# Kernel tuning notes

Hardware: AMD Instinct MI355X
Metric: run time of the kernel (lower is better)

Reference implementation:

```python
import jax, jax.numpy as jnp
import numpy as np

NUM_HEADS = 12

def quick_gelu(z):
    return z * jax.nn.sigmoid(1.702 * z)

def setup_inputs() -> dict:
    key = jax.random.key(0)
    ks = jax.random.split(key, 8)
    B, Fn, P, E, R = 16, 12, 197, 768, 8
    s = 0.02
    return {
        "x": jax.random.normal(ks[0], (B * Fn, P, E), jnp.float32),
        "in_proj_weight": jax.random.normal(ks[1], (3 * E, E), jnp.float32) * s,
        "in_proj_bias": jnp.zeros((3 * E,), jnp.float32),
        "out_proj_weight": jax.random.normal(ks[2], (E, E), jnp.float32) * s,
        "out_proj_bias": jnp.zeros((E,), jnp.float32),
        "lora_a": jax.random.normal(ks[3], (R, E), jnp.float32) * s,
        "lora_b": jax.random.normal(ks[4], (3 * E, R), jnp.float32) * s,
        "down_w": jax.random.normal(ks[5], (R, E), jnp.float32) * s,
        "down_b": jnp.zeros((R,), jnp.float32),
        "up_w": jax.random.normal(ks[6], (E, R), jnp.float32) * s,
        "up_b": jnp.zeros((E,), jnp.float32),
        "b": B, "n_f": Fn, "token_len": P, "d_v": E,
    }

def reference(x, in_proj_weight, in_proj_bias, out_proj_weight, out_proj_bias,
              lora_a, lora_b, down_w, down_b, up_w, up_b,
              b, n_f, token_len, d_v):
    bsz, tgt, E = x.shape
    h = NUM_HEADS
    hd = E // h
    scaling = float(hd) ** -0.5

    # fused qkv + LoRA delta: [bsz, tgt, 3E]
    qkv = x @ in_proj_weight.T + in_proj_bias
    qkv = qkv + (x @ lora_a.T) @ lora_b.T
    qkv = qkv.reshape(bsz, tgt, 3, h, hd).transpose(2, 0, 3, 1, 4)
    q, k, v = qkv[0], qkv[1], qkv[2]  # each [bsz, h, tgt, hd]

    # CLS-token query per frame: (b f) h p d -> b h f d  (p=0)
    q_1 = q.reshape(b, n_f, h, tgt, hd).transpose(0, 2, 1, 3, 4)[:, :, :, 0, :]

    # per-frame local attention
    attn = jax.nn.softmax((scaling * q) @ k.transpose(0, 1, 3, 2), axis=-1)
    out = (attn @ v).transpose(0, 2, 1, 3).reshape(bsz, tgt, E)
    out = out @ out_proj_weight.T + out_proj_bias

    # cross-frame kv: (b f) h p d -> b h (f p) d
    k_all = k.reshape(b, n_f, h, tgt, hd).transpose(0, 2, 1, 3, 4).reshape(b, h, n_f * tgt, hd)
    v_all = v.reshape(b, n_f, h, tgt, hd).transpose(0, 2, 1, 3, 4).reshape(b, h, n_f * tgt, hd)

    attn_1 = jax.nn.softmax((scaling * q_1) @ k_all.transpose(0, 1, 3, 2), axis=-1)
    x_1 = (attn_1 @ v_all).transpose(0, 2, 1, 3).reshape(b, n_f, E)
    x_1 = x_1 @ out_proj_weight.T + out_proj_bias

    out = out.reshape(b, n_f, token_len, d_v)
    x_0 = out[:, :, 0, :]
    x_0 = quick_gelu(x_0 @ down_w.T + down_b) @ up_w.T + up_b
    out = out.at[:, :, 0, :].set(x_0 + x_1)
    return out.reshape(b * n_f, token_len, d_v)
```

## Files before the change

kernel.cpp:

```cpp
#include <hip/hip_runtime.h>
#include <hip/hip_bf16.h>

typedef __hip_bfloat16 bf16;
typedef __attribute__((ext_vector_type(8))) short bf16x8;
typedef __attribute__((ext_vector_type(4))) float f32x4;

#define NT   37824
#define MPAD 37888
#define EDIM 768
#define N3   2304
#define TP   197
#define NB   16
#define NF   12
#define NH   12
#define HD   64
#define SCALE 0.125f
#define KALL 2364

__device__ __forceinline__ float bits2f(unsigned short u) {
    unsigned int v = ((unsigned int)u) << 16;
    return __uint_as_float(v);
}
__device__ __forceinline__ float b2f(bf16 v) { return __bfloat162float(v); }

__device__ __forceinline__ unsigned short bhi(float x) {
    union { bf16 b; unsigned short u; } cv; cv.b = __float2bfloat16(x); return cv.u;
}
__device__ __forceinline__ unsigned short blo(float x, unsigned short h) {
    float hf = __uint_as_float(((unsigned int)h) << 16);
    union { bf16 b; unsigned short u; } cv; cv.b = __float2bfloat16(x - hf); return cv.u;
}

__device__ __forceinline__ void storeC(float* p, float v) { *p = v; }
__device__ __forceinline__ void storeC(bf16* p, float v) { *p = __float2bfloat16(v); }

__device__ __forceinline__ void gload_lds16(const bf16* g, bf16* l) {
    __builtin_amdgcn_global_load_lds(
        (const __attribute__((address_space(1))) void*)g,
        (__attribute__((address_space(3))) void*)l,
        16, 0, 0);
}

__global__ __launch_bounds__(256) void lora_mid_kernel(const float* __restrict__ x,
        const float* __restrict__ la, float* __restrict__ mid) {
    int t = blockIdx.x * 4 + (threadIdx.x >> 6);
    int lane = threadIdx.x & 63;
    if (t >= NT) return;
    float acc[8];
#pragma unroll
    for (int r = 0; r < 8; r++) acc[r] = 0.f;
    const float* xr = x + (size_t)t * EDIM;
    for (int e = lane; e < EDIM; e += 64) {
        float xv = xr[e];
#pragma unroll
        for (int r = 0; r < 8; r++) acc[r] += xv * la[r * EDIM + e];
    }
#pragma unroll
    for (int r = 0; r < 8; r++) {
        float v = acc[r];
#pragma unroll
        for (int off = 32; off >= 1; off >>= 1) v += __shfl_xor(v, off, 64);
        if (lane == 0) mid[(size_t)t * 8 + r] = v;
    }
}

__global__ __launch_bounds__(256) void split_w_kernel(const float* __restrict__ w,
        bf16* __restrict__ o, int rows) {
    int idx = blockIdx.x * 256 + threadIdx.x;
    int total = rows * 192;
    if (idx >= total) return;
    int r = idx / 192, c = (idx - r * 192) * 4;
    float4 v = *reinterpret_cast<const float4*>(w + (size_t)r * 768 + c);
    ushort4 hi, lo;
    hi.x = bhi(v.x); hi.y = bhi(v.y); hi.z = bhi(v.z); hi.w = bhi(v.w);
    lo.x = blo(v.x, hi.x); lo.y = blo(v.y, hi.y); lo.z = blo(v.z, hi.z); lo.w = blo(v.w, hi.w);
    *(ushort4*)(o + (size_t)r * 1536 + c) = hi;
    *(ushort4*)(o + (size_t)r * 1536 + 768 + c) = lo;
}

template <typename OT, bool LORA>
__global__ __launch_bounds__(256) void mfma_gemm_kernel(const bf16* __restrict__ A, int lda,
        const bf16* __restrict__ W, const float* __restrict__ bias,
        const float* __restrict__ mid, const float* __restrict__ lb,
        OT* __restrict__ C, int M, int N, int KV) {
    __shared__ bf16 As[128 * 64];
    __shared__ bf16 Bs[128 * 64];
    const int tid = threadIdx.x;
    const int w = tid >> 6, lane = tid & 63;
    const int lr = lane & 15, lg = lane >> 4;
    const int wr = w >> 1, wc = w & 1;

    const int gx = gridDim.x;
    const int nwg = gx * gridDim.y;
    const int flat = blockIdx.y * gx + blockIdx.x;
    const int cpx = nwg >> 3;
    const int lid = (flat & 7) * cpx + (flat >> 3);
    const int m0 = (lid / gx) * 128, n0 = (lid % gx) * 128;

    f32x4 acc[4][4];
#pragma unroll
    for (int i = 0; i < 4; i++)
#pragma unroll
        for (int j = 0; j < 4; j++) acc[i][j] = (f32x4){0.f, 0.f, 0.f, 0.f};

    const int brs = lane >> 3;
    const int bcsw = ((lane & 7) ^ brs) << 3;

    for (int k0 = 0; k0 < KV; k0 += 64) {
        const int aOff = (k0 >= 768) ? k0 - 768 : k0;
        const int wOff = (k0 >= 1536) ? k0 - 1536 : k0;
        __syncthreads();
#pragma unroll
        for (int j = 0; j < 4; j++) {
            int seg = j * 4 + w;
            int row = seg * 8 + brs;
            gload_lds16(A + (size_t)(m0 + row) * lda + aOff + bcsw, &As[seg * 512]);
            gload_lds16(W + (size_t)(n0 + row) * 1536 + wOff + bcsw, &Bs[seg * 512]);
        }
        __syncthreads();
        bf16x8 a[4][2], b[4][2];
#pragma unroll
        for (int mf = 0; mf < 4; mf++) {
            int row = wr * 64 + mf * 16 + lr;
            int sw = (row & 7) << 4;
            a[mf][0] = *(const bf16x8*)((const char*)As + row * 128 + ((lg * 16) ^ sw));
            a[mf][1] = *(const bf16x8*)((const char*)As + row * 128 + ((64 + lg * 16) ^ sw));
        }
#pragma unroll
        for (int nf = 0; nf < 4; nf++) {
            int row = wc * 64 + nf * 16 + lr;
            int sw = (row & 7) << 4;
            b[nf][0] = *(const bf16x8*)((const char*)Bs + row * 128 + ((lg * 16) ^ sw));
            b[nf][1] = *(const bf16x8*)((const char*)Bs + row * 128 + ((64 + lg * 16) ^ sw));
        }
#pragma unroll
        for (int mf = 0; mf < 4; mf++)
#pragma unroll
            for (int nf = 0; nf < 4; nf++) {
                acc[mf][nf] = __builtin_amdgcn_mfma_f32_16x16x32_bf16(a[mf][0], b[nf][0], acc[mf][nf], 0, 0, 0);
                acc[mf][nf] = __builtin_amdgcn_mfma_f32_16x16x32_bf16(a[mf][1], b[nf][1], acc[mf][nf], 0, 0, 0);
            }
    }
#pragma unroll
    for (int mf = 0; mf < 4; mf++) {
#pragma unroll
        for (int r = 0; r < 4; r++) {
            int m = m0 + wr * 64 + mf * 16 + lg * 4 + r;
            if (m < M) {
                float mr[8];
                if constexpr (LORA) {
                    float4 u0 = *reinterpret_cast<const float4*>(mid + (size_t)m * 8);
                    float4 u1 = *reinterpret_cast<const float4*>(mid + (size_t)m * 8 + 4);
                    mr[0] = u0.x; mr[1] = u0.y; mr[2] = u0.z; mr[3] = u0.w;
                    mr[4] = u1.x; mr[5] = u1.y; mr[6] = u1.z; mr[7] = u1.w;
                }
#pragma unroll
                for (int nf = 0; nf < 4; nf++) {
                    int n = n0 + wc * 64 + nf * 16 + lr;
                    float v = acc[mf][nf][r] + bias[n];
                    if constexpr (LORA) {
                        const float4 l0 = *reinterpret_cast<const float4*>(lb + (size_t)n * 8);
                        const float4 l1 = *reinterpret_cast<const float4*>(lb + (size_t)n * 8 + 4);
                        v += mr[0] * l0.x + mr[1] * l0.y + mr[2] * l0.z + mr[3] * l0.w
                           + mr[4] * l1.x + mr[5] * l1.y + mr[6] * l1.z + mr[7] * l1.w;
                    }
                    storeC(C + (size_t)m * N + n, v);
                }
            }
        }
    }
}

__global__ __launch_bounds__(256) void attn_kernel(const bf16* __restrict__ qkv,
        bf16* __restrict__ ao) {
    __shared__ bf16 Ks[208 * 64];
    __shared__ bf16 Vt[64 * 208];
    __shared__ bf16 Ps[4][16 * 208];
    const int bb = blockIdx.x / NH;
    const int h = blockIdx.x % NH;
    const bf16* base = qkv + (size_t)bb * TP * N3;
    const int tid = threadIdx.x;
    const int w = tid >> 6, lane = tid & 63;
    const int lr = lane & 15, lg = lane >> 4;

    for (int idx = tid; idx < 208 * 16; idx += 256) {
        int row = idx >> 4, d4 = (idx & 15) * 4;
        ushort4 v = make_ushort4(0, 0, 0, 0);
        if (row < TP)
            v = *(const ushort4*)(base + (size_t)row * N3 + EDIM + h * 64 + d4);
        *(ushort4*)((char*)Ks + ((row * 128 + d4 * 2) ^ ((row & 7) << 4))) = v;
    }
    for (int g = w; g < 52; g += 4) {
        int kk0 = g * 4;
        int d = lane;
        const bf16* vb = base + (size_t)kk0 * N3 + 2 * EDIM + h * 64 + d;
        unsigned short t0 = 0, t1 = 0, t2 = 0, t3 = 0;
        if (kk0 + 0 < TP) t0 = *(const unsigned short*)(vb);
        if (kk0 + 1 < TP) t1 = *(const unsigned short*)(vb + N3);
        if (kk0 + 2 < TP) t2 = *(const unsigned short*)(vb + 2 * N3);
        if (kk0 + 3 < TP) t3 = *(const unsigned short*)(vb + 3 * N3);
        ushort4 v; v.x = t0; v.y = t1; v.z = t2; v.w = t3;
        *(ushort4*)((char*)Vt + ((d * 416 + kk0 * 2) ^ ((d & 7) << 4))) = v;
    }
    __syncthreads();

    bf16* Pw = &Ps[w][0];

    for (int qt = w; qt < 13; qt += 4) {
        int q = qt * 16 + lr; if (q > TP - 1) q = TP - 1;
        const bf16* qp = base + (size_t)q * N3 + h * 64 + lg * 8;
        bf16x8 qa0 = *(const bf16x8*)qp;
        bf16x8 qa1 = *(const bf16x8*)(qp + 32);

        f32x4 sf[13];
#pragma unroll
        for (int f = 0; f < 13; f++) {
            int row = f * 16 + lr;
            int swz = (row & 7) << 4;
            bf16x8 kb0 = *(const bf16x8*)((const char*)Ks + ((row * 128 + lg * 16) ^ swz));
            bf16x8 kb1 = *(const bf16x8*)((const char*)Ks + ((row * 128 + 64 + lg * 16) ^ swz));
            f32x4 c = {0.f, 0.f, 0.f, 0.f};
            c = __builtin_amdgcn_mfma_f32_16x16x32_bf16(qa0, kb0, c, 0, 0, 0);
            c = __builtin_amdgcn_mfma_f32_16x16x32_bf16(qa1, kb1, c, 0, 0, 0);
            sf[f] = c;
        }

        float mx[4] = {-1e30f, -1e30f, -1e30f, -1e30f};
#pragma unroll
        for (int f = 0; f < 13; f++) {
#pragma unroll
            for (int r = 0; r < 4; r++) {
                float s = sf[f][r] * SCALE;
                if (f == 12 && lr >= 5) s = -1e30f;
                sf[f][r] = s;
                mx[r] = fmaxf(mx[r], s);
            }
        }
#pragma unroll
        for (int off = 8; off >= 1; off >>= 1) {
#pragma unroll
            for (int r = 0; r < 4; r++) mx[r] = fmaxf(mx[r], __shfl_xor(mx[r], off, 64));
        }
        float lsum[4] = {0.f, 0.f, 0.f, 0.f};
#pragma unroll
        for (int f = 0; f < 13; f++) {
#pragma unroll
            for (int r = 0; r < 4; r++) {
                float e = __expf(sf[f][r] - mx[r]);
                sf[f][r] = e;
                lsum[r] += e;
            }
        }
#pragma unroll
        for (int off = 8; off >= 1; off >>= 1) {
#pragma unroll
            for (int r = 0; r < 4; r++) lsum[r] += __shfl_xor(lsum[r], off, 64);
        }
        float inv[4];
#pragma unroll
        for (int r = 0; r < 4; r++) inv[r] = 1.f / lsum[r];

#pragma unroll
        for (int f = 0; f < 13; f++) {
#pragma unroll
            for (int r = 0; r < 4; r++) {
                int row = lg * 4 + r;
                int col = f * 16 + lr;
                *(bf16*)((char*)Pw + ((row * 416 + col * 2) ^ ((row & 7) << 4))) =
                    __float2bfloat16(sf[f][r]);
            }
        }

        f32x4 of[4];
#pragma unroll
        for (int dt = 0; dt < 4; dt++) of[dt] = (f32x4){0.f, 0.f, 0.f, 0.f};
#pragma unroll
        for (int ks = 0; ks < 7; ks++) {
            int k0 = ks * 32 + lg * 8;
            bool ok = (k0 < 208);
            bf16x8 pa = {0, 0, 0, 0, 0, 0, 0, 0};
            if (ok)
                pa = *(const bf16x8*)((const char*)Pw + ((lr * 416 + k0 * 2) ^ ((lr & 7) << 4)));
#pragma unroll
            for (int dt = 0; dt < 4; dt++) {
                bf16x8 vb = {0, 0, 0, 0, 0, 0, 0, 0};
                if (ok) {
                    int d = dt * 16 + lr;
                    vb = *(const bf16x8*)((const char*)Vt + ((d * 416 + k0 * 2) ^ ((d & 7) << 4)));
                }
                of[dt] = __builtin_amdgcn_mfma_f32_16x16x32_bf16(pa, vb, of[dt], 0, 0, 0);
            }
        }

#pragma unroll
        for (int dt = 0; dt < 4; dt++) {
#pragma unroll
            for (int r = 0; r < 4; r++) {
                int qq = qt * 16 + lg * 4 + r;
                if (qq < TP)
                    ao[((size_t)bb * TP + qq) * EDIM + h * 64 + dt * 16 + lr] =
                        __float2bfloat16(of[dt][r] * inv[r]);
            }
        }
    }
}

__global__ __launch_bounds__(256) void xattn_kernel(const bf16* __restrict__ qkv,
        float* __restrict__ x1p) {
    __shared__ float q1[NF][64];
    __shared__ bf16 Ks[128][64];
    __shared__ bf16 Vs[128][64];
    __shared__ float sc[NF][128];
    __shared__ float Oacc[NF][64];
    __shared__ float mrow[NF], lrow[NF], arow[NF];
    const int b = blockIdx.x / NH, h = blockIdx.x % NH;
    const int tid = threadIdx.x;
    for (int idx = tid; idx < NF * 64; idx += 256) {
        int f = idx >> 6, d = idx & 63;
        q1[f][d] = b2f(qkv[(size_t)((b * NF + f) * TP) * N3 + h * 64 + d]);
        Oacc[f][d] = 0.f;
    }
    if (tid < NF) { mrow[tid] = -1e30f; lrow[tid] = 0.f; }
    __syncthreads();
    const int w = tid >> 6, lane = tid & 63;
    for (int kk0 = 0; kk0 < KALL; kk0 += 128) {
        for (int idx = tid; idx < 128 * 16; idx += 256) {
            int r = idx >> 4, d4 = (idx & 15) * 4;
            int kk = kk0 + r;
            if (kk < KALL) {
                int f = kk / TP, pp = kk - f * TP;
                const bf16* src = qkv + (size_t)((b * NF + f) * TP + pp) * N3 + h * 64 + d4;
                *(ushort4*)&Ks[r][d4] = *(const ushort4*)(src + 768);
                *(ushort4*)&Vs[r][d4] = *(const ushort4*)(src + 1536);
            } else {
                ushort4 z; z.x = z.y = z.z = z.w = 0;
                *(ushort4*)&Ks[r][d4] = z;
                *(ushort4*)&Vs[r][d4] = z;
            }
        }
        __syncthreads();
        for (int idx = tid; idx < NF * 128; idx += 256) {
            int f = idx >> 7, r = idx & 127;
            float s = -1e30f;
            if (kk0 + r < KALL) {
                const bf16* kr = &Ks[r][0];
                float a = 0.f;
#pragma unroll
                for (int d2 = 0; d2 < 32; d2++) {
                    unsigned int u = *reinterpret_cast<const unsigned int*>(kr + 2 * d2);
                    a += q1[f][2 * d2] * __uint_as_float(u << 16);
                    a += q1[f][2 * d2 + 1] * __uint_as_float(u & 0xffff0000u);
                }
                s = a * SCALE;
            }
            sc[f][r] = s;
        }
        __syncthreads();
        for (int qi = 0; qi < 3; qi++) {
            int f = qi * 4 + w;
            float s0 = sc[f][lane], s1v = sc[f][lane + 64];
            float mx = fmaxf(s0, s1v);
#pragma unroll
            for (int off = 32; off >= 1; off >>= 1) mx = fmaxf(mx, __shfl_xor(mx, off, 64));
            float mold = mrow[f];
            float mnew = fmaxf(mold, mx);
            float e0 = __expf(s0 - mnew), e1 = __expf(s1v - mnew);
            float ls = e0 + e1;
#pragma unroll
            for (int off = 32; off >= 1; off >>= 1) ls += __shfl_xor(ls, off, 64);
            sc[f][lane] = e0; sc[f][lane + 64] = e1;
            if (lane == 0) {
                float alpha = __expf(mold - mnew);
                arow[f] = alpha;
                lrow[f] = lrow[f] * alpha + ls;
                mrow[f] = mnew;
            }
        }
        __syncthreads();
        for (int idx = tid; idx < NF * 64; idx += 256) {
            int f = idx >> 6, d = idx & 63;
            float o = Oacc[f][d] * arow[f];
#pragma unroll 4
            for (int r = 0; r < 128; r++)
                o += sc[f][r] * b2f(Vs[r][d]);
            Oacc[f][d] = o;
        }
        __syncthreads();
    }
    for (int idx = tid; idx < NF * 64; idx += 256) {
        int f = idx >> 6, d = idx & 63;
        x1p[(size_t)(b * NF + f) * EDIM + h * 64 + d] = Oacc[f][d] / lrow[f];
    }
}

__global__ __launch_bounds__(256) void cls_kernel(float* __restrict__ out,
        const float* __restrict__ x1p, const float* __restrict__ Wout, const float* __restrict__ ob,
        const float* __restrict__ dw, const float* __restrict__ db,
        const float* __restrict__ uw, const float* __restrict__ ub) {
    __shared__ float x0s[EDIM], x1s[EDIM], gs[8];
    const int bfi = blockIdx.x;
    float* row = out + (size_t)bfi * TP * EDIM;
    const int tid = threadIdx.x;
    for (int i = tid; i < EDIM; i += 256) {
        x0s[i] = row[i];
        x1s[i] = x1p[(size_t)bfi * EDIM + i];
    }
    __syncthreads();
    {
        int r = tid >> 5, sl = tid & 31;
        float pr = 0.f;
        for (int e = sl; e < EDIM; e += 32) pr += x0s[e] * dw[r * EDIM + e];
#pragma unroll
        for (int off = 16; off >= 1; off >>= 1) pr += __shfl_xor(pr, off, 64);
        if (sl == 0) gs[r] = pr + db[r];
    }
    __syncthreads();
    float act[8];
#pragma unroll
    for (int r = 0; r < 8; r++) { float g = gs[r]; act[r] = g / (1.f + __expf(-1.702f * g)); }
    for (int j = tid; j < EDIM; j += 256) {
        float y = ub[j] + ob[j];
        const float4 u0 = *reinterpret_cast<const float4*>(uw + (size_t)j * 8);
        const float4 u1 = *reinterpret_cast<const float4*>(uw + (size_t)j * 8 + 4);
        y += act[0] * u0.x + act[1] * u0.y + act[2] * u0.z + act[3] * u0.w
           + act[4] * u1.x + act[5] * u1.y + act[6] * u1.z + act[7] * u1.w;
        const float* wr = Wout + (size_t)j * EDIM;
        float s = 0.f;
        for (int e = 0; e < EDIM; e += 4) {
            float4 wv = *reinterpret_cast<const float4*>(wr + e);
            s += x1s[e] * wv.x + x1s[e + 1] * wv.y + x1s[e + 2] * wv.z + x1s[e + 3] * wv.w;
        }
        y += s;
        row[j] = y;
    }
}

extern "C" void kernel_launch(void* const* d_in, const int* in_sizes, int n_in,
                              void* d_out, int out_size, void* d_ws, size_t ws_size,
                              hipStream_t stream) {
    (void)in_sizes; (void)n_in; (void)out_size; (void)ws_size;
    const float* x   = (const float*)d_in[0];
    const float* ipw = (const float*)d_in[1];
    const float* ipb = (const float*)d_in[2];
    const float* opw = (const float*)d_in[3];
    const float* opb = (const float*)d_in[4];
    const float* la  = (const float*)d_in[5];
    const float* lb  = (const float*)d_in[6];
    const float* dw  = (const float*)d_in[7];
    const float* db  = (const float*)d_in[8];
    const float* uw  = (const float*)d_in[9];
    const float* ub  = (const float*)d_in[10];
    float* out = (float*)d_out;

    char* wsb = (char*)d_ws;
    bf16* qkv = (bf16*)wsb;                       wsb += (size_t)NT * N3 * sizeof(bf16);
    bf16* ao  = (bf16*)wsb;                       wsb += (size_t)MPAD * EDIM * sizeof(bf16);
    bf16* xs  = (bf16*)wsb;                       wsb += (size_t)MPAD * 1536 * sizeof(bf16);
    bf16* W1  = (bf16*)wsb;                       wsb += (size_t)N3 * 1536 * sizeof(bf16);
    bf16* W2  = (bf16*)wsb;                       wsb += (size_t)EDIM * 1536 * sizeof(bf16);
    float* mid = (float*)wsb;                     wsb += (size_t)NT * 8 * sizeof(float);
    float* x1p = (float*)wsb;                     wsb += (size_t)NB * NF * EDIM * sizeof(float);

    split_w_kernel<<<(N3 * 192 + 255) / 256, 256, 0, stream>>>(ipw, W1, N3);
    split_w_kernel<<<(EDIM * 192 + 255) / 256, 256, 0, stream>>>(opw, W2, EDIM);
    split_w_kernel<<<(NT * 192 + 255) / 256, 256, 0, stream>>>(x, xs, NT);
    lora_mid_kernel<<<NT / 4, 256, 0, stream>>>(x, la, mid);
    mfma_gemm_kernel<bf16, true><<<dim3(N3 / 128, MPAD / 128), 256, 0, stream>>>(
        xs, 1536, W1, ipb, mid, lb, qkv, NT, N3, 2304);
    attn_kernel<<<192 * NH, 256, 0, stream>>>(qkv, ao);
    xattn_kernel<<<NB * NH, 256, 0, stream>>>(qkv, x1p);
    mfma_gemm_kernel<float, false><<<dim3(EDIM / 128, MPAD / 128), 256, 0, stream>>>(
        ao, 768, W2, opb, nullptr, nullptr, out, NT, EDIM, 1536);
    cls_kernel<<<NB * NF, 256, 0, stream>>>(out, x1p, opw, opb, dw, db, uw, ub);
}
```

Measured before the change: 1.558 ms.

## Double-buffer LDS tiles in MFMA GEMM to overlap global loads with compute

The GEMM kernel now uses two LDS buffers for the A and W tiles. It issues the async global-to-LDS loads for the next K tile before computing on the current one, which removes one of the two barriers per iteration. It also raises wave priority around the MFMA block. The aim is to hide global-load latency behind MFMA work, at the cost of double the LDS (64KB per block), which may lower occupancy.

```diff
diff --git a/kernel.cpp b/kernel.cpp
--- a/kernel.cpp
+++ b/kernel.cpp
@@ -83,8 +83,8 @@
         const bf16* __restrict__ W, const float* __restrict__ bias,
         const float* __restrict__ mid, const float* __restrict__ lb,
         OT* __restrict__ C, int M, int N, int KV) {
-    __shared__ bf16 As[128 * 64];
-    __shared__ bf16 Bs[128 * 64];
+    __shared__ bf16 As[2][128 * 64];
+    __shared__ bf16 Bs[2][128 * 64];
     const int tid = threadIdx.x;
     const int w = tid >> 6, lane = tid & 63;
     const int lr = lane & 15, lg = lane >> 4;
@@ -106,33 +106,51 @@
     const int brs = lane >> 3;
     const int bcsw = ((lane & 7) ^ brs) << 3;
 
-    for (int k0 = 0; k0 < KV; k0 += 64) {
-        const int aOff = (k0 >= 768) ? k0 - 768 : k0;
-        const int wOff = (k0 >= 1536) ? k0 - 1536 : k0;
-        __syncthreads();
+    const int nt = KV / 64;
+
+    {
+        const int aOff = 0, wOff = 0;
 #pragma unroll
         for (int j = 0; j < 4; j++) {
             int seg = j * 4 + w;
             int row = seg * 8 + brs;
-            gload_lds16(A + (size_t)(m0 + row) * lda + aOff + bcsw, &As[seg * 512]);
-            gload_lds16(W + (size_t)(n0 + row) * 1536 + wOff + bcsw, &Bs[seg * 512]);
-        }
-        __syncthreads();
+            gload_lds16(A + (size_t)(m0 + row) * lda + aOff + bcsw, &As[0][seg * 512]);
+            gload_lds16(W + (size_t)(n0 + row) * 1536 + wOff + bcsw, &Bs[0][seg * 512]);
+        }
+    }
+    __syncthreads();
+
+    int cur = 0;
+    for (int t = 0; t < nt; ++t) {
+        if (t + 1 < nt) {
+            const int k0 = (t + 1) * 64;
+            const int aOff = (k0 >= 768) ? k0 - 768 : k0;
+            const int wOff = (k0 >= 1536) ? k0 - 1536 : k0;
+            const int nxt = cur ^ 1;
+#pragma unroll
+            for (int j = 0; j < 4; j++) {
+                int seg = j * 4 + w;
+                int row = seg * 8 + brs;
+                gload_lds16(A + (size_t)(m0 + row) * lda + aOff + bcsw, &As[nxt][seg * 512]);
+                gload_lds16(W + (size_t)(n0 + row) * 1536 + wOff + bcsw, &Bs[nxt][seg * 512]);
+            }
+        }
         bf16x8 a[4][2], b[4][2];
 #pragma unroll
         for (int mf = 0; mf < 4; mf++) {
             int row = wr * 64 + mf * 16 + lr;
             int sw = (row & 7) << 4;
-            a[mf][0] = *(const bf16x8*)((const char*)As + row * 128 + ((lg * 16) ^ sw));
-            a[mf][1] = *(const bf16x8*)((const char*)As + row * 128 + ((64 + lg * 16) ^ sw));
+            a[mf][0] = *(const bf16x8*)((const char*)&As[cur][0] + row * 128 + ((lg * 16) ^ sw));
+            a[mf][1] = *(const bf16x8*)((const char*)&As[cur][0] + row * 128 + ((64 + lg * 16) ^ sw));
         }
 #pragma unroll
         for (int nf = 0; nf < 4; nf++) {
             int row = wc * 64 + nf * 16 + lr;
             int sw = (row & 7) << 4;
-            b[nf][0] = *(const bf16x8*)((const char*)Bs + row * 128 + ((lg * 16) ^ sw));
-            b[nf][1] = *(const bf16x8*)((const char*)Bs + row * 128 + ((64 + lg * 16) ^ sw));
-        }
+            b[nf][0] = *(const bf16x8*)((const char*)&Bs[cur][0] + row * 128 + ((lg * 16) ^ sw));
+            b[nf][1] = *(const bf16x8*)((const char*)&Bs[cur][0] + row * 128 + ((64 + lg * 16) ^ sw));
+        }
+        __builtin_amdgcn_s_setprio(1);
 #pragma unroll
         for (int mf = 0; mf < 4; mf++)
 #pragma unroll
@@ -140,6 +158,9 @@
                 acc[mf][nf] = __builtin_amdgcn_mfma_f32_16x16x32_bf16(a[mf][0], b[nf][0], acc[mf][nf], 0, 0, 0);
                 acc[mf][nf] = __builtin_amdgcn_mfma_f32_16x16x32_bf16(a[mf][1], b[nf][1], acc[mf][nf], 0, 0, 0);
             }
+        __builtin_amdgcn_s_setprio(0);
+        __syncthreads();
+        cur ^= 1;
     }
 #pragma unroll
     for (int mf = 0; mf < 4; mf++) {
```

After: 1.541 ms. About the same (-1.1%).
